# Performance work log

Measured on AMD Instinct MI355X. Metric: run time of the kernel, lower is better.

## Reference

```python
import jax, jax.numpy as jnp
import numpy as np

B, L, D = 4, 512, 768
NUM_SPANS = 4096
MAX_WIDTH = 8
DFF = 4 * D


def setup_inputs() -> dict:
    key = jax.random.key(0)
    k_h, k_s, k_w, k1, k2 = jax.random.split(key, 5)
    h = jax.random.normal(k_h, (B, L, D), dtype=jnp.float32)
    starts = jax.random.randint(k_s, (B, NUM_SPANS), 0, L)
    widths = jax.random.randint(k_w, (B, NUM_SPANS), 1, MAX_WIDTH + 1)
    ends = jnp.minimum(starts + widths - 1, L - 1)
    span_idx = jnp.stack([starts, ends], axis=-1).astype(jnp.int64 if jax.config.jax_enable_x64 else jnp.int32)
    W1 = jax.random.normal(k1, (D, DFF), dtype=jnp.float32) * (1.0 / np.sqrt(D))
    b1 = jnp.zeros((DFF,), dtype=jnp.float32)
    W2 = jax.random.normal(k2, (DFF, D), dtype=jnp.float32) * (1.0 / np.sqrt(DFF))
    b2 = jnp.zeros((D,), dtype=jnp.float32)
    return {"h": h, "span_idx": span_idx, "W1": W1, "b1": b1, "W2": W2, "b2": b2,
            "max_width": MAX_WIDTH}


def reference(h, span_idx, W1, b1, W2, b2, max_width):
    # h: [B, L, D]; span_idx: [B, S, 2] (start, end inclusive)
    Bv, Lv, Dv = h.shape
    starts = span_idx[:, :, 0]                       # [B, S]
    lengths = span_idx[:, :, 1] - starts + 1         # [B, S]
    offsets = jnp.arange(max_width)                  # static bound on span length
    positions = starts[:, :, None] + offsets[None, None, :]      # [B, S, W]
    mask = offsets[None, None, :] < lengths[:, :, None]          # [B, S, W]
    positions = jnp.clip(positions * mask, 0, Lv - 1)
    # indexed gather-reduce (no [B,S,L,D] broadcast): [B, S, W, D]
    gathered = h[jnp.arange(Bv)[:, None, None], positions]
    summed = jnp.sum(gathered * mask[..., None].astype(h.dtype), axis=2)  # [B, S, D]
    span_reps = summed / lengths[..., None].astype(h.dtype)
    # projection: Linear -> ReLU -> (Dropout: identity at eval) -> Linear
    hmid = jax.nn.relu(jnp.einsum('bsd,df->bsf', span_reps, W1) + b1)
    out = jnp.einsum('bsf,fd->bsd', hmid, W2) + b2
    return out
```

## Files before the change

kernel.cpp:

```cpp
#include <hip/hip_runtime.h>
#include <stdint.h>

#define B_DIM 4
#define L_DIM 512
#define D_DIM 768
#define S_DIM 4096
#define DFF_DIM 3072
#define M_DIM (B_DIM * S_DIM)

typedef unsigned short ushort_t;
typedef __attribute__((ext_vector_type(8))) short short8;
typedef __attribute__((ext_vector_type(4))) float floatx4;

__device__ __forceinline__ ushort_t f2bf(float x) {
  unsigned int u = __float_as_uint(x);
  u += 0x7FFFu + ((u >> 16) & 1u);
  return (ushort_t)(u >> 16);
}

__device__ __forceinline__ void load_lds16(const ushort_t* g, ushort_t* lds) {
  __builtin_amdgcn_global_load_lds(
      (const __attribute__((address_space(1))) unsigned int*)g,
      (__attribute__((address_space(3))) unsigned int*)lds, 16, 0, 0);
}

__global__ __launch_bounds__(256)
void transpose_bf16(const float* __restrict__ in, ushort_t* __restrict__ out,
                    int K, int N) {
  __shared__ float tile[32][33];
  const int k0 = blockIdx.x * 32;
  const int n0 = blockIdx.y * 32;
  const int tx = threadIdx.x & 31;
  const int ty = threadIdx.x >> 5;
#pragma unroll
  for (int r = 0; r < 32; r += 8)
    tile[ty + r][tx] = in[(long)(k0 + ty + r) * N + n0 + tx];
  __syncthreads();
#pragma unroll
  for (int r = 0; r < 32; r += 8)
    out[(long)(n0 + ty + r) * K + k0 + tx] = f2bf(tile[tx][ty + r]);
}

__global__ __launch_bounds__(256)
void span_reps(const float* __restrict__ h, const int* __restrict__ span_idx,
               ushort_t* __restrict__ A) {
  const int wave = threadIdx.x >> 6;
  const int lane = threadIdx.x & 63;
  const int span = blockIdx.x * 4 + wave;
  const int b = span >> 12;
  const int start = span_idx[span * 2 + 0];
  const int end   = span_idx[span * 2 + 1];
  const float inv = 1.0f / (float)(end - start + 1);
  const float* hb = h + ((long)b * L_DIM + start) * D_DIM + lane;
  float a[12];
#pragma unroll
  for (int c = 0; c < 12; ++c) a[c] = 0.0f;
  for (int p = start; p <= end; ++p) {
#pragma unroll
    for (int c = 0; c < 12; ++c) a[c] += hb[c * 64];
    hb += D_DIM;
  }
  ushort_t* o = A + (long)span * D_DIM + lane;
#pragma unroll
  for (int c = 0; c < 12; ++c) o[c * 64] = f2bf(a[c] * inv);
}

template <int MODE>
__global__ __launch_bounds__(256)
void gemm_bt(const ushort_t* __restrict__ A, const ushort_t* __restrict__ Bt,
             const float* __restrict__ bias, void* __restrict__ Cv,
             int M, int N, int K) {
  __shared__ ushort_t As[2][128 * 32];
  __shared__ ushort_t Bs[2][128 * 32];

  const int tid  = threadIdx.x;
  const int lane = tid & 63;
  const int wave = tid >> 6;
  const int l16  = lane & 15;
  const int quad = lane >> 4;

  const int bn = blockIdx.x;
  const int bm = blockIdx.y;

  const int wm = (wave & 1) * 64;
  const int wn = (wave >> 1) * 64;

  floatx4 acc[4][4];
#pragma unroll
  for (int i = 0; i < 4; ++i)
#pragma unroll
    for (int j = 0; j < 4; ++j)
      acc[i][j] = (floatx4)0.0f;

  const int s0 = tid, s1 = tid + 256;
  const ushort_t* gA0 = A + (long)(bm * 128 + (s0 >> 2)) * K + (s0 & 3) * 8;
  const ushort_t* gA1 = A + (long)(bm * 128 + (s1 >> 2)) * K + (s1 & 3) * 8;
  const ushort_t* gB0 = Bt + (long)(bn * 128 + (s0 >> 2)) * K + (s0 & 3) * 8;
  const ushort_t* gB1 = Bt + (long)(bn * 128 + (s1 >> 2)) * K + (s1 & 3) * 8;

  const int nk = K >> 5;

  load_lds16(gA0, &As[0][0] + s0 * 8);
  load_lds16(gA1, &As[0][0] + s1 * 8);
  load_lds16(gB0, &Bs[0][0] + s0 * 8);
  load_lds16(gB1, &Bs[0][0] + s1 * 8);

  for (int k = 0; k < nk; ++k) {
    const int cur = k & 1;
    const int nxt = cur ^ 1;
    __syncthreads();

    if (k + 1 < nk) {
      const int off = (k + 1) * 32;
      load_lds16(gA0 + off, &As[nxt][0] + s0 * 8);
      load_lds16(gA1 + off, &As[nxt][0] + s1 * 8);
      load_lds16(gB0 + off, &Bs[nxt][0] + s0 * 8);
      load_lds16(gB1 + off, &Bs[nxt][0] + s1 * 8);
    }

    short8 af[4], bf[4];
#pragma unroll
    for (int i = 0; i < 4; ++i)
      af[i] = *(const short8*)(&As[cur][0] + (wm + i * 16 + l16) * 32 + quad * 8);
#pragma unroll
    for (int j = 0; j < 4; ++j)
      bf[j] = *(const short8*)(&Bs[cur][0] + (wn + j * 16 + l16) * 32 + quad * 8);
#pragma unroll
    for (int i = 0; i < 4; ++i)
#pragma unroll
      for (int j = 0; j < 4; ++j)
        acc[i][j] = __builtin_amdgcn_mfma_f32_16x16x32_bf16(af[i], bf[j], acc[i][j], 0, 0, 0);
  }

#pragma unroll
  for (int i = 0; i < 4; ++i) {
#pragma unroll
    for (int j = 0; j < 4; ++j) {
      const int col = bn * 128 + wn + j * 16 + l16;
      const float bv = bias[col];
      const int row0 = bm * 128 + wm + i * 16 + quad * 4;
#pragma unroll
      for (int r = 0; r < 4; ++r) {
        float v = acc[i][j][r] + bv;
        if (MODE == 0) {
          v = v > 0.0f ? v : 0.0f;
          ((ushort_t*)Cv)[(long)(row0 + r) * N + col] = f2bf(v);
        } else {
          ((float*)Cv)[(long)(row0 + r) * N + col] = v;
        }
      }
    }
  }
}

extern "C" void kernel_launch(void* const* d_in, const int* in_sizes, int n_in,
                              void* d_out, int out_size, void* d_ws, size_t ws_size,
                              hipStream_t stream) {
  const float* h        = (const float*)d_in[0];
  const int*   span_idx = (const int*)d_in[1];
  const float* W1       = (const float*)d_in[2];
  const float* b1       = (const float*)d_in[3];
  const float* W2       = (const float*)d_in[4];
  const float* b2       = (const float*)d_in[5];
  float* out = (float*)d_out;

  ushort_t* A   = (ushort_t*)d_ws;
  ushort_t* W1T = A + (size_t)M_DIM * D_DIM;
  ushort_t* W2T = W1T + (size_t)DFF_DIM * D_DIM;
  ushort_t* Hm  = W2T + (size_t)D_DIM * DFF_DIM;

  transpose_bf16<<<dim3(D_DIM / 32, DFF_DIM / 32), 256, 0, stream>>>(W1, W1T, D_DIM, DFF_DIM);
  transpose_bf16<<<dim3(DFF_DIM / 32, D_DIM / 32), 256, 0, stream>>>(W2, W2T, DFF_DIM, D_DIM);

  span_reps<<<M_DIM / 4, 256, 0, stream>>>(h, span_idx, A);

  gemm_bt<0><<<dim3(DFF_DIM / 128, M_DIM / 128), 256, 0, stream>>>(
      A, W1T, b1, Hm, M_DIM, DFF_DIM, D_DIM);

  gemm_bt<1><<<dim3(D_DIM / 128, M_DIM / 128), 256, 0, stream>>>(
      Hm, W2T, b2, out, M_DIM, D_DIM, DFF_DIM);
}
```

Baseline: 315.1 us.

## Fuse prep kernels, XOR-swizzle GEMM LDS layout, and swap block raster order

Merges the two weight transposes and the span-mean kernel into one launch, which saves launch overhead and lets the pieces run concurrently. In the GEMM, each thread's global-to-LDS load picks a permuted 16-byte chunk column, and the fragment reads use the matching XOR offset, to reduce LDS bank conflicts on the short8 reads. It also swaps grid x/y so consecutive blocks walk along M with the same N tile, which changes L2 reuse of weights versus activations.

Result: faster. 279.2 us (-11.4%).

```diff
diff --git a/kernel.cpp b/kernel.cpp
--- a/kernel.cpp
+++ b/kernel.cpp
@@ -24,12 +24,12 @@
       (__attribute__((address_space(3))) unsigned int*)lds, 16, 0, 0);
 }
 
-__global__ __launch_bounds__(256)
-void transpose_bf16(const float* __restrict__ in, ushort_t* __restrict__ out,
-                    int K, int N) {
+__device__ __forceinline__ void transpose_body(const float* __restrict__ in,
+                                               ushort_t* __restrict__ out,
+                                               int K, int N, int kb, int nb) {
   __shared__ float tile[32][33];
-  const int k0 = blockIdx.x * 32;
-  const int n0 = blockIdx.y * 32;
+  const int k0 = kb * 32;
+  const int n0 = nb * 32;
   const int tx = threadIdx.x & 31;
   const int ty = threadIdx.x >> 5;
 #pragma unroll
@@ -41,12 +41,12 @@
     out[(long)(n0 + ty + r) * K + k0 + tx] = f2bf(tile[tx][ty + r]);
 }
 
-__global__ __launch_bounds__(256)
-void span_reps(const float* __restrict__ h, const int* __restrict__ span_idx,
-               ushort_t* __restrict__ A) {
+__device__ __forceinline__ void span_body(const float* __restrict__ h,
+                                          const int* __restrict__ span_idx,
+                                          ushort_t* __restrict__ A, int blk) {
   const int wave = threadIdx.x >> 6;
   const int lane = threadIdx.x & 63;
-  const int span = blockIdx.x * 4 + wave;
+  const int span = blk * 4 + wave;
   const int b = span >> 12;
   const int start = span_idx[span * 2 + 0];
   const int end   = span_idx[span * 2 + 1];
@@ -63,6 +63,22 @@
   ushort_t* o = A + (long)span * D_DIM + lane;
 #pragma unroll
   for (int c = 0; c < 12; ++c) o[c * 64] = f2bf(a[c] * inv);
+}
+
+__global__ __launch_bounds__(256)
+void prep(const float* __restrict__ W1, ushort_t* __restrict__ W1T,
+          const float* __restrict__ W2, ushort_t* __restrict__ W2T,
+          const float* __restrict__ h, const int* __restrict__ span_idx,
+          ushort_t* __restrict__ A) {
+  const int blk = blockIdx.x;
+  if (blk < 2304) {
+    transpose_body(W1, W1T, D_DIM, DFF_DIM, blk % 24, blk / 24);
+  } else if (blk < 4608) {
+    const int b = blk - 2304;
+    transpose_body(W2, W2T, DFF_DIM, D_DIM, b % 96, b / 96);
+  } else {
+    span_body(h, span_idx, A, blk - 4608);
+  }
 }
 
 template <int MODE>
@@ -79,12 +95,15 @@
   const int l16  = lane & 15;
   const int quad = lane >> 4;
 
-  const int bn = blockIdx.x;
-  const int bm = blockIdx.y;
+  const int bm = blockIdx.x;
+  const int bn = blockIdx.y;
 
   const int wm = (wave & 1) * 64;
   const int wn = (wave >> 1) * 64;
 
+  const int swz  = (l16 & 3) ^ ((l16 >> 2) & 3);
+  const int coff = (quad ^ swz) * 8;
+
   floatx4 acc[4][4];
 #pragma unroll
   for (int i = 0; i < 4; ++i)
@@ -93,10 +112,13 @@
       acc[i][j] = (floatx4)0.0f;
 
   const int s0 = tid, s1 = tid + 256;
-  const ushort_t* gA0 = A + (long)(bm * 128 + (s0 >> 2)) * K + (s0 & 3) * 8;
-  const ushort_t* gA1 = A + (long)(bm * 128 + (s1 >> 2)) * K + (s1 & 3) * 8;
-  const ushort_t* gB0 = Bt + (long)(bn * 128 + (s0 >> 2)) * K + (s0 & 3) * 8;
-  const ushort_t* gB1 = Bt + (long)(bn * 128 + (s1 >> 2)) * K + (s1 & 3) * 8;
+  const int r0 = s0 >> 2, r1 = s1 >> 2;
+  const int c0 = (s0 & 3) ^ (r0 & 3) ^ ((r0 >> 2) & 3);
+  const int c1 = (s1 & 3) ^ (r1 & 3) ^ ((r1 >> 2) & 3);
+  const ushort_t* gA0 = A + (long)(bm * 128 + r0) * K + c0 * 8;
+  const ushort_t* gA1 = A + (long)(bm * 128 + r1) * K + c1 * 8;
+  const ushort_t* gB0 = Bt + (long)(bn * 128 + r0) * K + c0 * 8;
+  const ushort_t* gB1 = Bt + (long)(bn * 128 + r1) * K + c1 * 8;
 
   const int nk = K >> 5;
 
@@ -121,10 +143,10 @@
     short8 af[4], bf[4];
 #pragma unroll
     for (int i = 0; i < 4; ++i)
-      af[i] = *(const short8*)(&As[cur][0] + (wm + i * 16 + l16) * 32 + quad * 8);
+      af[i] = *(const short8*)(&As[cur][0] + (wm + i * 16 + l16) * 32 + coff);
 #pragma unroll
     for (int j = 0; j < 4; ++j)
-      bf[j] = *(const short8*)(&Bs[cur][0] + (wn + j * 16 + l16) * 32 + quad * 8);
+      bf[j] = *(const short8*)(&Bs[cur][0] + (wn + j * 16 + l16) * 32 + coff);
 #pragma unroll
     for (int i = 0; i < 4; ++i)
 #pragma unroll
@@ -169,14 +191,11 @@
   ushort_t* W2T = W1T + (size_t)DFF_DIM * D_DIM;
   ushort_t* Hm  = W2T + (size_t)D_DIM * DFF_DIM;
 
-  transpose_bf16<<<dim3(D_DIM / 32, DFF_DIM / 32), 256, 0, stream>>>(W1, W1T, D_DIM, DFF_DIM);
-  transpose_bf16<<<dim3(DFF_DIM / 32, D_DIM / 32), 256, 0, stream>>>(W2, W2T, DFF_DIM, D_DIM);
-
-  span_reps<<<M_DIM / 4, 256, 0, stream>>>(h, span_idx, A);
-
-  gemm_bt<0><<<dim3(DFF_DIM / 128, M_DIM / 128), 256, 0, stream>>>(
+  prep<<<2304 + 2304 + M_DIM / 4, 256, 0, stream>>>(W1, W1T, W2, W2T, h, span_idx, A);
+
+  gemm_bt<0><<<dim3(M_DIM / 128, DFF_DIM / 128), 256, 0, stream>>>(
       A, W1T, b1, Hm, M_DIM, DFF_DIM, D_DIM);
 
-  gemm_bt<1><<<dim3(D_DIM / 128, M_DIM / 128), 256, 0, stream>>>(
+  gemm_bt<1><<<dim3(M_DIM / 128, D_DIM / 128), 256, 0, stream>>>(
       Hm, W2T, b2, out, M_DIM, D_DIM, DFF_DIM);
 }
```
